# Performance work log

Hardware: AMD Instinct MI355X
Metric: run time of the kernel (lower is better)

## Reference

```python
import jax, jax.numpy as jnp
import numpy as np

EPS = 1e-5      # InstanceNorm2d default eps
SLOPE = 0.2     # leaky relu negative_slope
K = 16          # neighbors
C = 128         # feature_dim


def _knn_idx(coords, k):
    # coords: [B,3,N] -> idx [B,N,k] of k nearest neighbors (excluding self)
    x = jnp.transpose(coords, (0, 2, 1))            # [B,N,3]
    sq = jnp.sum(x * x, axis=-1)                    # [B,N]
    dist = sq[:, :, None] + sq[:, None, :] - 2.0 * jnp.einsum('bnd,bmd->bnm', x, x)
    _, idx = jax.lax.top_k(-dist, k + 1)            # smallest distances, sorted
    return idx[:, :, 1:]                            # drop self


def _graph_feature(feats, idx):
    # feats: [B,C,N], idx: [B,N,k] -> [B,2C,N,k] = cat(center, neighbor-center)
    neigh = jax.vmap(lambda f, i: f[:, i])(feats, idx)   # [B,C,N,k]
    center = feats[:, :, :, None]
    return jnp.concatenate(
        [jnp.broadcast_to(center, neigh.shape), neigh - center], axis=1)


def _inorm(x):
    # InstanceNorm2d (affine=False): normalize each (b,c) over spatial dims
    mean = jnp.mean(x, axis=(2, 3), keepdims=True)
    var = jnp.mean((x - mean) ** 2, axis=(2, 3), keepdims=True)
    return (x - mean) * jax.lax.rsqrt(var + EPS)


def _edge_block(x, W):
    # 1x1 conv (W: [O,I]) + instance norm + leaky relu, x: [B,I,N,k]
    h = jnp.einsum('oi,bink->bonk', W, x)
    return jax.nn.leaky_relu(_inorm(h), SLOPE)


def setup_inputs() -> dict:
    key = jax.random.key(0)
    k1, k2, k3, k4, k5 = jax.random.split(key, 5)
    B, N = 2, 8192
    coords = jax.random.normal(k1, (B, 3, N), dtype=jnp.float32)
    features = jax.random.normal(k2, (B, C, N), dtype=jnp.float32)
    W1 = jax.random.normal(k3, (C, 2 * C), dtype=jnp.float32) * 0.05
    W2 = jax.random.normal(k4, (2 * C, 2 * C), dtype=jnp.float32) * 0.05
    W3 = jax.random.normal(k5, (C, 4 * C), dtype=jnp.float32) * 0.05
    return {"coords": coords, "features": features, "W1": W1, "W2": W2, "W3": W3}


def reference(coords, features, W1, W2, W3):
    idx = _knn_idx(coords, K)                       # [B,N,K]
    x0 = features                                   # [B,C,N]
    # block 1: EdgeConv C -> C
    x1 = _edge_block(_graph_feature(x0, idx), W1)   # [B,C,N,K]
    x1 = jnp.max(x1, axis=-1)                       # [B,C,N]
    # block 2: EdgeConv C -> 2C (same coords => same knn indices)
    x2 = _edge_block(_graph_feature(x1, idx), W2)   # [B,2C,N,K]
    x2 = jnp.max(x2, axis=-1)                       # [B,2C,N]
    # fuse: 1x1 conv 4C -> C + instance norm (over N) + leaky relu
    x3 = jnp.concatenate([x0, x1, x2], axis=1)      # [B,4C,N]
    h = jnp.einsum('oi,bin->bon', W3, x3)           # [B,C,N]
    h = _inorm(h[:, :, :, None])[:, :, :, 0]
    return jax.nn.leaky_relu(h, SLOPE)
```

## Files before the change

### kernel.cpp

```cpp
#include <hip/hip_runtime.h>
#include <hip/hip_bf16.h>
#include <cstdint>
#include <cstddef>

#define B_ 2
#define N_ 8192
#define C_ 128
#define K_ 16
#define NK_ (N_ * K_)
#define EPS_ 1e-5f
#define SLOPE_ 0.2f
#define INF_ 3.0e38f

typedef __attribute__((ext_vector_type(8))) short short8;
typedef __attribute__((ext_vector_type(4))) float f32x4;

static constexpr size_t OFF_IDX   = 0x000000;
static constexpr size_t OFF_CPK   = 0x100000;
static constexpr size_t OFF_CPK64 = 0x140000;
static constexpr size_t OFF_ACC   = 0x1C0000;
static constexpr size_t OFF_WC1   = 0x1D0000;
static constexpr size_t OFF_WC2   = 0x1E0000;
static constexpr size_t OFF_WB3   = 0x200000;
static constexpr size_t OFF_X3T   = 0x240000;
static constexpr size_t OFF_PQ    = OFF_X3T + (size_t)B_ * N_ * 512 * 2;

__device__ __forceinline__ __hip_bfloat16 ftob(float f) { return __float2bfloat16(f); }
__device__ __forceinline__ float bf2f(unsigned short h) {
  unsigned u = ((unsigned)h) << 16;
  return __uint_as_float(u);
}
__device__ __forceinline__ short f2bs(float f) {
  __hip_bfloat16 h = __float2bfloat16(f);
  return *reinterpret_cast<short*>(&h);
}

__global__ void prep_kernel(const float* __restrict__ coords,
                            const float* __restrict__ W1,
                            const float* __restrict__ W2,
                            const float* __restrict__ W3,
                            __hip_bfloat16* __restrict__ wc1, __hip_bfloat16* __restrict__ wc2,
                            __hip_bfloat16* __restrict__ wb3,
                            float4* __restrict__ cpk, double4* __restrict__ cpk64,
                            float* __restrict__ acc) {
  int tid = blockIdx.x * 256 + threadIdx.x;
  if (tid < 32768) {
    int o = tid >> 7, i = tid & 127;
    float v;
    if (o < 128) v = W1[o * 256 + i] - W1[o * 256 + 128 + i];
    else         v = W1[(o - 128) * 256 + 128 + i];
    wc1[tid] = ftob(v);
  } else if (tid < 32768 + 65536) {
    int t2 = tid - 32768;
    int o = t2 >> 7, i = t2 & 127;
    float v;
    if (o < 256) v = W2[o * 256 + i] - W2[o * 256 + 128 + i];
    else         v = W2[(o - 256) * 256 + 128 + i];
    wc2[t2] = ftob(v);
  } else if (tid < 98304 + 65536) {
    int t2 = tid - 98304;
    wb3[t2] = ftob(W3[t2]);
  } else if (tid < 163840 + B_ * N_) {
    int q = tid - 163840;
    int b = q >> 13, n = q & (N_ - 1);
    float x = coords[(b * 3 + 0) * N_ + n];
    float y = coords[(b * 3 + 1) * N_ + n];
    float z = coords[(b * 3 + 2) * N_ + n];
    float sq = __fadd_rn(__fadd_rn(__fmul_rn(x, x), __fmul_rn(y, y)), __fmul_rn(z, z));
    cpk[q] = make_float4(x, y, z, sq);
    double xd = (double)x, yd = (double)y, zd = (double)z;
    double sqd = (xd * xd + yd * yd) + zd * zd;
    cpk64[q] = make_double4(xd, yd, zd, sqd);
  } else if (tid < 180224 + 2048) {
    acc[tid - 180224] = 0.f;
  }
}

__global__ __launch_bounds__(256) void transpose_kernel(const float* __restrict__ x0,
                                                        __hip_bfloat16* __restrict__ x3t) {
  __shared__ float tile[64 * 68];
  int b = blockIdx.z, c0 = blockIdx.y * 64, n0 = blockIdx.x * 64;
  int t = threadIdx.x;
  int r = t >> 4;
  int c4 = (t & 15) * 4;
#pragma unroll
  for (int i = 0; i < 4; ++i) {
    int row = r + i * 16;
    float4 v = *(const float4*)&x0[((size_t)(b * C_ + c0 + row)) * N_ + n0 + c4];
    *(float4*)&tile[row * 68 + c4] = v;
  }
  __syncthreads();
#pragma unroll
  for (int i = 0; i < 4; ++i) {
    int nl = r + i * 16;
    __hip_bfloat16* dst = &x3t[((size_t)(b * N_ + n0 + nl)) * 512 + c0 + c4];
    dst[0] = ftob(tile[(c4 + 0) * 68 + nl]);
    dst[1] = ftob(tile[(c4 + 1) * 68 + nl]);
    dst[2] = ftob(tile[(c4 + 2) * 68 + nl]);
    dst[3] = ftob(tile[(c4 + 3) * 68 + nl]);
  }
}

__device__ __forceinline__ float thresh17(float v, int lane) {
#pragma unroll
  for (int k2 = 2; k2 <= 64; k2 <<= 1) {
#pragma unroll
    for (int j = k2 >> 1; j > 0; j >>= 1) {
      float o = __shfl_xor(v, j, 64);
      bool up = ((lane & k2) == 0);
      bool lower = ((lane & j) == 0);
      v = ((lower == up)) ? fminf(v, o) : fmaxf(v, o);
    }
  }
  return __shfl(v, 16, 64);
}

__device__ __forceinline__ void bsort64d(double& d, int& ix, int lane) {
#pragma unroll
  for (int k2 = 2; k2 <= 64; k2 <<= 1) {
#pragma unroll
    for (int j = k2 >> 1; j > 0; j >>= 1) {
      double od = __shfl_xor(d, j, 64);
      int oi = __shfl_xor(ix, j, 64);
      bool up = ((lane & k2) == 0);
      bool lower = ((lane & j) == 0);
      bool takeMin = (lower == up);
      bool less = (od < d) || (od == d && oi < ix);
      if (takeMin == less) { d = od; ix = oi; }
    }
  }
}

__global__ __launch_bounds__(256) void knn_kernel(const float4* __restrict__ cpk,
                                                  const double4* __restrict__ cpk64,
                                                  int* __restrict__ idxout) {
  __shared__ float4 ctile[512];
  __shared__ int scnt[4][4];
  __shared__ int sii[4][4][128];
  int t = threadIdx.x;
  int lane = t & 63;
  int wv = t >> 6;
  int q0 = (blockIdx.x * 4 + wv) * 4;
  int b = q0 >> 13;
  const float4* cb = cpk + (size_t)b * N_;
  const double4* cb64 = cpk64 + (size_t)b * N_;
  float4 me0 = cpk[q0], me1 = cpk[q0 + 1], me2 = cpk[q0 + 2], me3 = cpk[q0 + 3];
  float a0x = -2.f * me0.x, a0y = -2.f * me0.y, a0z = -2.f * me0.z;
  float a1x = -2.f * me1.x, a1y = -2.f * me1.y, a1z = -2.f * me1.z;
  float a2x = -2.f * me2.x, a2y = -2.f * me2.y, a2z = -2.f * me2.z;
  float a3x = -2.f * me3.x, a3y = -2.f * me3.y, a3z = -2.f * me3.z;

  if (lane < 4) scnt[wv][lane] = 0;

  float m0 = INF_, m1 = INF_, m2 = INF_, m3 = INF_;
  for (int tb = 0; tb < 16; ++tb) {
    __syncthreads();
    ctile[t] = cb[tb * 512 + t];
    ctile[t + 256] = cb[tb * 512 + 256 + t];
    __syncthreads();
#pragma unroll
    for (int i = 0; i < 8; ++i) {
      float4 c = ctile[i * 64 + lane];
      m0 = fminf(m0, fmaf(a0z, c.z, fmaf(a0y, c.y, fmaf(a0x, c.x, c.w))));
      m1 = fminf(m1, fmaf(a1z, c.z, fmaf(a1y, c.y, fmaf(a1x, c.x, c.w))));
      m2 = fminf(m2, fmaf(a2z, c.z, fmaf(a2y, c.y, fmaf(a2x, c.x, c.w))));
      m3 = fminf(m3, fmaf(a3z, c.z, fmaf(a3y, c.y, fmaf(a3x, c.x, c.w))));
    }
  }
  float T0 = thresh17(m0, lane) + 1e-3f;
  float T1 = thresh17(m1, lane) + 1e-3f;
  float T2 = thresh17(m2, lane) + 1e-3f;
  float T3 = thresh17(m3, lane) + 1e-3f;

  for (int tb = 0; tb < 16; ++tb) {
    __syncthreads();
    ctile[t] = cb[tb * 512 + t];
    ctile[t + 256] = cb[tb * 512 + 256 + t];
    __syncthreads();
#pragma unroll
    for (int i = 0; i < 8; ++i) {
      float4 c = ctile[i * 64 + lane];
      float p0 = fmaf(a0z, c.z, fmaf(a0y, c.y, fmaf(a0x, c.x, c.w)));
      float p1 = fmaf(a1z, c.z, fmaf(a1y, c.y, fmaf(a1x, c.x, c.w)));
      float p2 = fmaf(a2z, c.z, fmaf(a2y, c.y, fmaf(a2x, c.x, c.w)));
      float p3 = fmaf(a3z, c.z, fmaf(a3y, c.y, fmaf(a3x, c.x, c.w)));
      bool h0 = p0 <= T0, h1 = p1 <= T1, h2 = p2 <= T2, h3 = p3 <= T3;
      if (h0 | h1 | h2 | h3) {
        int m = tb * 512 + i * 64 + lane;
        if (h0) { int p = atomicAdd(&scnt[wv][0], 1); if (p < 128) sii[wv][0][p] = m; }
        if (h1) { int p = atomicAdd(&scnt[wv][1], 1); if (p < 128) sii[wv][1][p] = m; }
        if (h2) { int p = atomicAdd(&scnt[wv][2], 1); if (p < 128) sii[wv][2][p] = m; }
        if (h3) { int p = atomicAdd(&scnt[wv][3], 1); if (p < 128) sii[wv][3][p] = m; }
      }
    }
  }
  __syncthreads();

#pragma unroll 1
  for (int j = 0; j < 4; ++j) {
    int q = q0 + j;
    int n = q & (N_ - 1);
    int cnt = scnt[wv][j] < 128 ? scnt[wv][j] : 128;
    double4 me64 = cb64[n];
    double d1 = 1e300; int ix1 = 0x7FFFFFFF;
    if (lane < cnt) {
      int m = sii[wv][j][lane];
      if (m != n) {
        double4 c = cb64[m];
        double dot = (me64.x * c.x + me64.y * c.y) + me64.z * c.z;
        d1 = (me64.w + c.w) - 2.0 * dot;
        ix1 = m;
      }
    }
    bsort64d(d1, ix1, lane);
    if (cnt > 64) {
      double d2 = 1e300; int ix2 = 0x7FFFFFFF;
      if (lane + 64 < cnt) {
        int m = sii[wv][j][lane + 64];
        if (m != n) {
          double4 c = cb64[m];
          double dot = (me64.x * c.x + me64.y * c.y) + me64.z * c.z;
          d2 = (me64.w + c.w) - 2.0 * dot;
          ix2 = m;
        }
      }
      bsort64d(d2, ix2, lane);
      int src = (lane - 16) & 63;
      double dB = __shfl(d2, src, 64);
      int iB = __shfl(ix2, src, 64);
      double nd = (lane < 16) ? d1 : ((lane < 32) ? dB : 1e300);
      int nix = (lane < 16) ? ix1 : ((lane < 32) ? iB : 0x7FFFFFFF);
      bsort64d(nd, nix, lane);
      d1 = nd; ix1 = nix;
    }
    if (lane < 16) idxout[(size_t)q * 16 + lane] = ix1;
  }
}

template <typename OUT, int NORM>
__global__ __launch_bounds__(256) void gemm_mfma(const __hip_bfloat16* __restrict__ X, int ldx,
                                                 const __hip_bfloat16* __restrict__ W, int ldw,
                                                 OUT* __restrict__ Cc, int ldc, int Ktot,
                                                 const float* __restrict__ nacc) {
  __shared__ short As[64 * 40];
  int b = blockIdx.z;
  int n0 = blockIdx.x * 64, o0 = blockIdx.y * 64;
  int t = threadIdx.x;
  int lane = t & 63, wv = t >> 6;
  int nh = (wv & 1) * 32, oh = (wv >> 1) * 32;
  const __hip_bfloat16* Xb = X + (size_t)(b * N_ + n0) * ldx;
  f32x4 acc00 = {0.f, 0.f, 0.f, 0.f}, acc01 = acc00, acc10 = acc00, acc11 = acc00;
  int sr = t >> 2;
  int sc = (t & 3) * 8;
  int arow = lane & 15;
  int kq = (lane >> 4) * 8;
  for (int kt = 0; kt < Ktot; kt += 32) {
    short8 av = *(const short8*)&Xb[(size_t)sr * ldx + kt + sc];
    if constexpr (NORM != 0) {
      int k = kt + sc;
      const float* pa = nullptr;
      if constexpr (NORM == 2) {
        if (k >= 128 && k < 256) pa = nacc + ((size_t)b * 128 + (k - 128)) * 2;
        else if (k >= 256)       pa = nacc + 512 + ((size_t)b * 256 + (k - 256)) * 2;
      } else {
        pa = nacc + ((size_t)b * 128 + k) * 2;
      }
      if (pa) {
        const float inv = 1.f / (float)NK_;
        short8 outv;
#pragma unroll
        for (int j = 0; j < 8; ++j) {
          float s1 = pa[2 * j], s2 = pa[2 * j + 1];
          float mean = s1 * inv;
          float var = fmaf(s2, inv, -mean * mean);
          float rs = rsqrtf(var + EPS_);
          float v = bf2f((unsigned short)av[j]);
          float y = (v - mean) * rs;
          y = y > 0.f ? y : SLOPE_ * y;
          outv[j] = f2bs(y);
        }
        av = outv;
      }
    }
    *(short8*)&As[sr * 40 + sc] = av;
    __syncthreads();
    short8 a0 = *(const short8*)&As[(nh + arow) * 40 + kq];
    short8 a1 = *(const short8*)&As[(nh + 16 + arow) * 40 + kq];
    const __hip_bfloat16* Wp = W + (size_t)(o0 + oh + arow) * ldw + kt + kq;
    short8 b0 = *(const short8*)&Wp[0];
    short8 b1 = *(const short8*)&Wp[16 * (size_t)ldw];
    acc00 = __builtin_amdgcn_mfma_f32_16x16x32_bf16(a0, b0, acc00, 0, 0, 0);
    acc01 = __builtin_amdgcn_mfma_f32_16x16x32_bf16(a0, b1, acc01, 0, 0, 0);
    acc10 = __builtin_amdgcn_mfma_f32_16x16x32_bf16(a1, b0, acc10, 0, 0, 0);
    acc11 = __builtin_amdgcn_mfma_f32_16x16x32_bf16(a1, b1, acc11, 0, 0, 0);
    __syncthreads();
  }
  int crow = (lane >> 4) * 4;
  int ccol = lane & 15;
#pragma unroll
  for (int r = 0; r < 4; ++r) {
    size_t row0 = (size_t)(b * N_ + n0 + nh + crow + r) * ldc + o0 + oh;
    size_t row1 = (size_t)(b * N_ + n0 + nh + 16 + crow + r) * ldc + o0 + oh;
    if constexpr (sizeof(OUT) == 4) {
      Cc[row0 + ccol]      = acc00[r];
      Cc[row0 + 16 + ccol] = acc01[r];
      Cc[row1 + ccol]      = acc10[r];
      Cc[row1 + 16 + ccol] = acc11[r];
    } else {
      Cc[row0 + ccol]      = ftob(acc00[r]);
      Cc[row0 + 16 + ccol] = ftob(acc01[r]);
      Cc[row1 + ccol]      = ftob(acc10[r]);
      Cc[row1 + 16 + ccol] = ftob(acc11[r]);
    }
  }
}

template <int CO>
__global__ __launch_bounds__(256) void edge_kernel(const __hip_bfloat16* __restrict__ PQ,
                                                   const int* __restrict__ idx,
                                                   __hip_bfloat16* __restrict__ Mout,
                                                   float* __restrict__ acc) {
  constexpr int CP = CO / 2;
  constexpr int NG = 256 / CP;
  __shared__ float r1a[256], r1b[256], r2a[256], r2b[256];
  int b = blockIdx.y;
  int n0 = blockIdx.x * 64;
  int t = threadIdx.x;
  int oc = t & (CP - 1);
  int o2 = oc * 2;
  int qg = t / CP;
  float s1a = 0.f, s1b = 0.f, s2a = 0.f, s2b = 0.f;
  const __hip_bfloat16* PQb = PQ + (size_t)b * N_ * (2 * CO);
  for (int qq = qg; qq < 64; qq += NG) {
    int n = n0 + qq;
    const int4* ip = (const int4*)&idx[(size_t)(b * N_ + n) * 16];
    int4 i0 = ip[0], i1 = ip[1], i2 = ip[2], i3 = ip[3];
    unsigned pu = *(const unsigned*)&PQb[(size_t)n * (2 * CO) + o2];
    float pa = bf2f((unsigned short)(pu & 0xFFFF));
    float pb = bf2f((unsigned short)(pu >> 16));
    float hma = -INF_, hmb = -INF_;
#define EDGE_STEP(mm)                                                         \
    { int mc = (mm) & (N_ - 1);                                               \
      unsigned vu = *(const unsigned*)&PQb[(size_t)mc * (2 * CO) + CO + o2];  \
      float ha = pa + bf2f((unsigned short)(vu & 0xFFFF));                    \
      float hb = pb + bf2f((unsigned short)(vu >> 16));                       \
      hma = fmaxf(hma, ha); s1a += ha; s2a = fmaf(ha, ha, s2a);               \
      hmb = fmaxf(hmb, hb); s1b += hb; s2b = fmaf(hb, hb, s2b); }
    EDGE_STEP(i0.x) EDGE_STEP(i0.y) EDGE_STEP(i0.z) EDGE_STEP(i0.w)
    EDGE_STEP(i1.x) EDGE_STEP(i1.y) EDGE_STEP(i1.z) EDGE_STEP(i1.w)
    EDGE_STEP(i2.x) EDGE_STEP(i2.y) EDGE_STEP(i2.z) EDGE_STEP(i2.w)
    EDGE_STEP(i3.x) EDGE_STEP(i3.y) EDGE_STEP(i3.z) EDGE_STEP(i3.w)
#undef EDGE_STEP
    __hip_bfloat162 hh;
    hh.x = ftob(hma); hh.y = ftob(hmb);
    *(__hip_bfloat162*)&Mout[(size_t)(b * N_ + n) * 512 + o2] = hh;
  }
  r1a[t] = s1a; r1b[t] = s1b; r2a[t] = s2a; r2b[t] = s2b;
  __syncthreads();
  if (t < CP) {
#pragma unroll
    for (int g = 1; g < NG; ++g) {
      s1a += r1a[t + g * CP]; s1b += r1b[t + g * CP];
      s2a += r2a[t + g * CP]; s2b += r2b[t + g * CP];
    }
    atomicAdd(&acc[(b * CO + o2) * 2 + 0], s1a);
    atomicAdd(&acc[(b * CO + o2) * 2 + 1], s2a);
    atomicAdd(&acc[(b * CO + o2 + 1) * 2 + 0], s1b);
    atomicAdd(&acc[(b * CO + o2 + 1) * 2 + 1], s2b);
  }
}

__global__ __launch_bounds__(256) void colred_kernel(const float* __restrict__ H,
                                                     float* __restrict__ acc3) {
  __shared__ float r1[256], r2[256];
  int b = blockIdx.y;
  int n0 = blockIdx.x * 32;
  int t = threadIdx.x;
  int o = t & 127, half = t >> 7;
  float s1 = 0.f, s2 = 0.f;
  for (int i = 0; i < 16; ++i) {
    int n = n0 + half * 16 + i;
    float v = H[(size_t)(b * N_ + n) * 128 + o];
    s1 += v; s2 = fmaf(v, v, s2);
  }
  r1[t] = s1; r2[t] = s2;
  __syncthreads();
  if (t < 128) {
    s1 = r1[t] + r1[t + 128];
    s2 = r2[t] + r2[t + 128];
    atomicAdd(&acc3[(b * 128 + o) * 2 + 0], s1);
    atomicAdd(&acc3[(b * 128 + o) * 2 + 1], s2);
  }
}

__global__ __launch_bounds__(256) void final_kernel(const float* __restrict__ H,
                                                    const float* __restrict__ acc3,
                                                    float* __restrict__ out) {
  __shared__ float tile[32 * 132];
  int b = blockIdx.y, n0 = blockIdx.x * 32;
  int t = threadIdx.x;
  int r = t >> 3;
  int c8 = t & 7;
#pragma unroll
  for (int i = 0; i < 4; ++i) {
    int col4 = (c8 + i * 8) * 4;
    *(float4*)&tile[r * 132 + col4] = *(const float4*)&H[(size_t)(b * N_ + n0 + r) * 128 + col4];
  }
  __syncthreads();
  int o = t >> 1;
  int nh = (t & 1) * 16;
  float s1 = acc3[(b * 128 + o) * 2], s2 = acc3[(b * 128 + o) * 2 + 1];
  const float inv = 1.f / (float)N_;
  float mean = s1 * inv;
  float var = fmaf(s2, inv, -mean * mean);
  float rs = rsqrtf(var + EPS_);
#pragma unroll
  for (int i = 0; i < 16; ++i) {
    int nl = nh + i;
    float v = tile[nl * 132 + o];
    float y = (v - mean) * rs;
    y = y > 0.f ? y : SLOPE_ * y;
    out[(size_t)(b * 128 + o) * N_ + n0 + nl] = y;
  }
}

extern "C" void kernel_launch(void* const* d_in, const int* in_sizes, int n_in,
                              void* d_out, int out_size, void* d_ws, size_t ws_size,
                              hipStream_t stream) {
  const float* coords = (const float*)d_in[0];
  const float* feats = (const float*)d_in[1];
  const float* W1 = (const float*)d_in[2];
  const float* W2 = (const float*)d_in[3];
  const float* W3 = (const float*)d_in[4];
  char* ws = (char*)d_ws;
  int* idx = (int*)(ws + OFF_IDX);
  float4* cpk = (float4*)(ws + OFF_CPK);
  double4* cpk64 = (double4*)(ws + OFF_CPK64);
  float* acc = (float*)(ws + OFF_ACC);
  __hip_bfloat16* wc1 = (__hip_bfloat16*)(ws + OFF_WC1);
  __hip_bfloat16* wc2 = (__hip_bfloat16*)(ws + OFF_WC2);
  __hip_bfloat16* wb3 = (__hip_bfloat16*)(ws + OFF_WB3);
  __hip_bfloat16* x3t = (__hip_bfloat16*)(ws + OFF_X3T);
  __hip_bfloat16* pqb = (__hip_bfloat16*)(ws + OFF_PQ);
  float* ht = (float*)(ws + OFF_PQ);

  prep_kernel<<<712, 256, 0, stream>>>(coords, W1, W2, W3, wc1, wc2, wb3, cpk, cpk64, acc);
  transpose_kernel<<<dim3(128, 2, 2), 256, 0, stream>>>(feats, x3t);
  knn_kernel<<<1024, 256, 0, stream>>>(cpk, cpk64, idx);
  gemm_mfma<__hip_bfloat16, 0><<<dim3(128, 4, 2), 256, 0, stream>>>(x3t, 512, wc1, 128, pqb, 256, 128, nullptr);
  edge_kernel<128><<<dim3(128, 2), 256, 0, stream>>>(pqb, idx, x3t + 128, acc + 0);
  gemm_mfma<__hip_bfloat16, 1><<<dim3(128, 8, 2), 256, 0, stream>>>(x3t + 128, 512, wc2, 128, pqb, 512, 128, acc);
  edge_kernel<256><<<dim3(128, 2), 256, 0, stream>>>(pqb, idx, x3t + 256, acc + 512);
  gemm_mfma<float, 2><<<dim3(128, 2, 2), 256, 0, stream>>>(x3t, 512, wb3, 512, ht, 128, 512, acc);
  colred_kernel<<<dim3(256, 2), 256, 0, stream>>>(ht, acc + 1536);
  final_kernel<<<dim3(256, 2), 256, 0, stream>>>(ht, acc + 1536, (float*)d_out);
}
```

Baseline: 212.4 us.

## Halve queries per wave in knn and double-buffer coordinate tiles

The knn kernel now handles 2 queries per wave instead of 4, so it launches twice as many blocks (2048). The coordinate tile is double-buffered in 256-entry halves with one barrier per tile instead of two. The aim is more parallelism and better latency hiding for the brute-force distance scan. In exchange, every block rereads the full coordinate set, so total LDS and global reads for coordinates double.

```diff
diff --git a/kernel.cpp b/kernel.cpp
--- a/kernel.cpp
+++ b/kernel.cpp
@@ -134,70 +134,61 @@
 __global__ __launch_bounds__(256) void knn_kernel(const float4* __restrict__ cpk,
                                                   const double4* __restrict__ cpk64,
                                                   int* __restrict__ idxout) {
-  __shared__ float4 ctile[512];
-  __shared__ int scnt[4][4];
-  __shared__ int sii[4][4][128];
+  __shared__ float4 ctile[2][256];
+  __shared__ int scnt[4][2];
+  __shared__ int sii[4][2][128];
   int t = threadIdx.x;
   int lane = t & 63;
   int wv = t >> 6;
-  int q0 = (blockIdx.x * 4 + wv) * 4;
+  int q0 = (blockIdx.x * 4 + wv) * 2;
   int b = q0 >> 13;
   const float4* cb = cpk + (size_t)b * N_;
   const double4* cb64 = cpk64 + (size_t)b * N_;
-  float4 me0 = cpk[q0], me1 = cpk[q0 + 1], me2 = cpk[q0 + 2], me3 = cpk[q0 + 3];
+  float4 me0 = cpk[q0], me1 = cpk[q0 + 1];
   float a0x = -2.f * me0.x, a0y = -2.f * me0.y, a0z = -2.f * me0.z;
   float a1x = -2.f * me1.x, a1y = -2.f * me1.y, a1z = -2.f * me1.z;
-  float a2x = -2.f * me2.x, a2y = -2.f * me2.y, a2z = -2.f * me2.z;
-  float a3x = -2.f * me3.x, a3y = -2.f * me3.y, a3z = -2.f * me3.z;
-
-  if (lane < 4) scnt[wv][lane] = 0;
-
-  float m0 = INF_, m1 = INF_, m2 = INF_, m3 = INF_;
-  for (int tb = 0; tb < 16; ++tb) {
-    __syncthreads();
-    ctile[t] = cb[tb * 512 + t];
-    ctile[t + 256] = cb[tb * 512 + 256 + t];
-    __syncthreads();
-#pragma unroll
-    for (int i = 0; i < 8; ++i) {
-      float4 c = ctile[i * 64 + lane];
+
+  if (lane < 2) scnt[wv][lane] = 0;
+
+  float m0 = INF_, m1 = INF_;
+  ctile[0][t] = cb[t];
+  __syncthreads();
+  for (int tb = 0; tb < 32; ++tb) {
+    if (tb + 1 < 32) ctile[(tb + 1) & 1][t] = cb[(tb + 1) * 256 + t];
+    const float4* cc = ctile[tb & 1];
+#pragma unroll
+    for (int i = 0; i < 4; ++i) {
+      float4 c = cc[i * 64 + lane];
       m0 = fminf(m0, fmaf(a0z, c.z, fmaf(a0y, c.y, fmaf(a0x, c.x, c.w))));
       m1 = fminf(m1, fmaf(a1z, c.z, fmaf(a1y, c.y, fmaf(a1x, c.x, c.w))));
-      m2 = fminf(m2, fmaf(a2z, c.z, fmaf(a2y, c.y, fmaf(a2x, c.x, c.w))));
-      m3 = fminf(m3, fmaf(a3z, c.z, fmaf(a3y, c.y, fmaf(a3x, c.x, c.w))));
-    }
+    }
+    __syncthreads();
   }
   float T0 = thresh17(m0, lane) + 1e-3f;
   float T1 = thresh17(m1, lane) + 1e-3f;
-  float T2 = thresh17(m2, lane) + 1e-3f;
-  float T3 = thresh17(m3, lane) + 1e-3f;
-
-  for (int tb = 0; tb < 16; ++tb) {
-    __syncthreads();
-    ctile[t] = cb[tb * 512 + t];
-    ctile[t + 256] = cb[tb * 512 + 256 + t];
-    __syncthreads();
-#pragma unroll
-    for (int i = 0; i < 8; ++i) {
-      float4 c = ctile[i * 64 + lane];
+
+  ctile[0][t] = cb[t];
+  __syncthreads();
+  for (int tb = 0; tb < 32; ++tb) {
+    if (tb + 1 < 32) ctile[(tb + 1) & 1][t] = cb[(tb + 1) * 256 + t];
+    const float4* cc = ctile[tb & 1];
+#pragma unroll
+    for (int i = 0; i < 4; ++i) {
+      float4 c = cc[i * 64 + lane];
       float p0 = fmaf(a0z, c.z, fmaf(a0y, c.y, fmaf(a0x, c.x, c.w)));
       float p1 = fmaf(a1z, c.z, fmaf(a1y, c.y, fmaf(a1x, c.x, c.w)));
-      float p2 = fmaf(a2z, c.z, fmaf(a2y, c.y, fmaf(a2x, c.x, c.w)));
-      float p3 = fmaf(a3z, c.z, fmaf(a3y, c.y, fmaf(a3x, c.x, c.w)));
-      bool h0 = p0 <= T0, h1 = p1 <= T1, h2 = p2 <= T2, h3 = p3 <= T3;
-      if (h0 | h1 | h2 | h3) {
-        int m = tb * 512 + i * 64 + lane;
+      bool h0 = p0 <= T0, h1 = p1 <= T1;
+      if (h0 | h1) {
+        int m = tb * 256 + i * 64 + lane;
         if (h0) { int p = atomicAdd(&scnt[wv][0], 1); if (p < 128) sii[wv][0][p] = m; }
         if (h1) { int p = atomicAdd(&scnt[wv][1], 1); if (p < 128) sii[wv][1][p] = m; }
-        if (h2) { int p = atomicAdd(&scnt[wv][2], 1); if (p < 128) sii[wv][2][p] = m; }
-        if (h3) { int p = atomicAdd(&scnt[wv][3], 1); if (p < 128) sii[wv][3][p] = m; }
       }
     }
-  }
-  __syncthreads();
+    __syncthreads();
+  }
 
 #pragma unroll 1
-  for (int j = 0; j < 4; ++j) {
+  for (int j = 0; j < 2; ++j) {
     int q = q0 + j;
     int n = q & (N_ - 1);
     int cnt = scnt[wv][j] < 128 ? scnt[wv][j] : 128;
@@ -446,7 +437,7 @@
 
   prep_kernel<<<712, 256, 0, stream>>>(coords, W1, W2, W3, wc1, wc2, wb3, cpk, cpk64, acc);
   transpose_kernel<<<dim3(128, 2, 2), 256, 0, stream>>>(feats, x3t);
-  knn_kernel<<<1024, 256, 0, stream>>>(cpk, cpk64, idx);
+  knn_kernel<<<2048, 256, 0, stream>>>(cpk, cpk64, idx);
   gemm_mfma<__hip_bfloat16, 0><<<dim3(128, 4, 2), 256, 0, stream>>>(x3t, 512, wc1, 128, pqb, 256, 128, nullptr);
   edge_kernel<128><<<dim3(128, 2), 256, 0, stream>>>(pqb, idx, x3t + 128, acc + 0);
   gemm_mfma<__hip_bfloat16, 1><<<dim3(128, 8, 2), 256, 0, stream>>>(x3t + 128, 512, wc2, 128, pqb, 512, 128, acc);
```

Result: slower. 228.5 us (+7.6%).
